# Performance work log

Measured on AMD Instinct MI355X. Metric: run time of the kernel, lower is better.

## Reference

```python
import jax, jax.numpy as jnp
import numpy as np

B, D, K, H, W = 2, 512, 32, 64, 64


def setup_inputs() -> dict:
    key = jax.random.key(0)
    k1, k2, k3 = jax.random.split(key, 3)
    X = jax.random.normal(k1, (B, D, H, W), dtype=jnp.float32)
    std1 = 1.0 / (K * D) ** 0.5
    codewords = jax.random.uniform(k2, (K, D), minval=-std1, maxval=std1, dtype=jnp.float32)
    scale = jax.random.uniform(k3, (D, K), minval=-1.0, maxval=0.0, dtype=jnp.float32)
    return {"X": X, "codewords": codewords, "scale": scale}


def reference(X, codewords, scale):
    # X: [B, D, H, W] -> x: [B, N, D], N = H*W
    Bv, Dv = X.shape[0], X.shape[1]
    x = X.reshape(Bv, Dv, -1).transpose(0, 2, 1)            # [B, N, D]
    # broadcast residual: x[b,n,d] - codewords[k,d], scaled per (d,k)
    residual = (x[:, :, :, None] - codewords.T) * scale     # [B, N, D, K]
    # soft assignment over K codewords
    Q = jax.nn.softmax(-0.5 * jnp.sum(residual * residual, axis=2), axis=2)  # [B, N, K]
    # weighted aggregation over N, normalized by per-codeword mass
    Z_num = jnp.einsum('bnk,bndk->bdk', Q, residual)        # [B, D, K]
    Z_ = Z_num / Q.sum(axis=1)[:, None, :]                  # [B, D, K]
    # L2-normalize along D
    Z = Z_ / jnp.sqrt(jnp.sum(Z_ * Z_, axis=1, keepdims=True))
    return (Z, Q)
```

## Files before the change

### kernel.cpp

```cpp
#include <hip/hip_runtime.h>
#include <math.h>

#define B_DIM 2
#define D_DIM 512
#define K_DIM 32
#define N_DIM 4096

__global__ __launch_bounds__(256, 2)
void k_dist_q(const float* __restrict__ X, const float* __restrict__ CW,
              const float* __restrict__ SC, float* __restrict__ Qout,
              float* __restrict__ nsq)
{
    __shared__ __align__(16) float xlds[16 * 516];
    __shared__ __align__(16) float red[16 * 16 * 36];

    const int tid = threadIdx.x;
    const int b  = blockIdx.x >> 8;
    const int n0 = (blockIdx.x & 255) << 4;
    const int dp = tid & 63;
    const int kp = tid >> 6;
    const int k0 = kp << 3;

    if (blockIdx.x == 0 && tid < 2 * K_DIM) nsq[tid] = 0.f;

    const float* xsrc = X + (size_t)b * D_DIM * N_DIM + n0;
#pragma unroll
    for (int j = 0; j < 8; ++j) {
        const int d  = (tid >> 2) + (j << 6);
        const int n4 = (tid & 3) << 2;
        float4 v = *(const float4*)(xsrc + (size_t)d * N_DIM + n4);
        xlds[(n4 + 0) * 516 + d] = v.x;
        xlds[(n4 + 1) * 516 + d] = v.y;
        xlds[(n4 + 2) * 516 + d] = v.z;
        xlds[(n4 + 3) * 516 + d] = v.w;
    }

    float cv[8][8];
#pragma unroll
    for (int kk = 0; kk < 8; ++kk) {
        const float* cr = CW + (k0 + kk) * D_DIM + (dp << 2);
        float4 c0 = *(const float4*)(cr);
        float4 c1 = *(const float4*)(cr + 256);
        cv[kk][0] = c0.x; cv[kk][1] = c0.y; cv[kk][2] = c0.z; cv[kk][3] = c0.w;
        cv[kk][4] = c1.x; cv[kk][5] = c1.y; cv[kk][6] = c1.z; cv[kk][7] = c1.w;
    }
    float Areg[8][8], Breg[8][8], ckp[8];
#pragma unroll
    for (int kk = 0; kk < 8; ++kk) ckp[kk] = 0.f;
#pragma unroll
    for (int dd = 0; dd < 8; ++dd) {
        const int d = (dd < 4) ? ((dp << 2) + dd) : (256 + (dp << 2) + (dd - 4));
        float4 s0 = *(const float4*)(SC + d * K_DIM + k0);
        float4 s1 = *(const float4*)(SC + d * K_DIM + k0 + 4);
        float sv[8] = {s0.x, s0.y, s0.z, s0.w, s1.x, s1.y, s1.z, s1.w};
#pragma unroll
        for (int kk = 0; kk < 8; ++kk) {
            float c = cv[kk][dd];
            float a = sv[kk] * sv[kk];
            Areg[dd][kk] = a;
            Breg[dd][kk] = -2.f * a * c;
            ckp[kk] = fmaf(a * c, c, ckp[kk]);
        }
    }
    __syncthreads();

#pragma unroll
    for (int n = 0; n < 16; ++n) {
        float dist[8];
#pragma unroll
        for (int kk = 0; kk < 8; ++kk) dist[kk] = ckp[kk];
        float4 xa = *(const float4*)(&xlds[n * 516 + (dp << 2)]);
        float4 xb = *(const float4*)(&xlds[n * 516 + (dp << 2) + 256]);
        float xv[8] = {xa.x, xa.y, xa.z, xa.w, xb.x, xb.y, xb.z, xb.w};
#pragma unroll
        for (int dd = 0; dd < 8; ++dd) {
            const float x  = xv[dd];
            const float x2 = x * x;
#pragma unroll
            for (int kk = 0; kk < 8; ++kk) {
                dist[kk] = fmaf(Areg[dd][kk], x2, dist[kk]);
                dist[kk] = fmaf(Breg[dd][kk], x,  dist[kk]);
            }
        }
#pragma unroll
        for (int kk = 0; kk < 8; ++kk) {
            dist[kk] += __shfl_xor(dist[kk], 32);
            dist[kk] += __shfl_xor(dist[kk], 16);
        }
        if (dp < 16) {
            float* r = &red[(n * 16 + dp) * 36 + k0];
            *(float4*)(r)     = make_float4(dist[0], dist[1], dist[2], dist[3]);
            *(float4*)(r + 4) = make_float4(dist[4], dist[5], dist[6], dist[7]);
        }
    }
    __syncthreads();

#pragma unroll
    for (int h = 0; h < 2; ++h) {
        const int n = (tid >> 5) + (h << 3);
        const int k = tid & 31;
        float dsum = 0.f;
#pragma unroll
        for (int i = 0; i < 16; ++i) dsum += red[(n * 16 + i) * 36 + k];
        float m = dsum;
#pragma unroll
        for (int mk = 16; mk >= 1; mk >>= 1)
            m = fminf(m, __shfl_xor(m, mk));
        float e = __expf(-0.5f * (dsum - m));
        float ssum = e;
#pragma unroll
        for (int mk = 16; mk >= 1; mk >>= 1)
            ssum += __shfl_xor(ssum, mk);
        Qout[((size_t)b * N_DIM + n0 + n) * K_DIM + k] = __fdividef(e, ssum);
    }
}

__global__ __launch_bounds__(256, 2)
void k_tpart(const float* __restrict__ X, const float* __restrict__ Qin,
             float* __restrict__ TP, float* __restrict__ Mpart)
{
    __shared__ __align__(16) float Xs[64 * 68];
    __shared__ __align__(16) float Qs[32 * 68];
    __shared__ __align__(16) float red4[4 * 64 * 36];
    __shared__ float mred[8][33];

    const int tid = threadIdx.x;
    const int bid = blockIdx.x;
    const int ns = bid & 31;
    const int dt = (bid >> 5) & 7;
    const int b  = bid >> 8;
    const int nsub = tid >> 5;
    const int dp = tid & 7;
    const int kp = (tid >> 3) & 3;
    const int wv = tid >> 6;

    float acc[8][8];
#pragma unroll
    for (int i = 0; i < 8; ++i)
#pragma unroll
        for (int j = 0; j < 8; ++j) acc[i][j] = 0.f;

    const float* xsrc = X + ((size_t)b * D_DIM + dt * 64) * N_DIM + ns * 128;
    const float* qsrc = Qin + ((size_t)b * N_DIM + ns * 128) * K_DIM;

    for (int ch = 0; ch < 2; ++ch) {
        __syncthreads();
#pragma unroll
        for (int i = 0; i < 4; ++i) {
            int flat4 = tid + (i << 8);
            int row = flat4 >> 4;
            int c4  = (flat4 & 15) << 2;
            float4 v = *(const float4*)(xsrc + (size_t)row * N_DIM + (ch << 6) + c4);
            *(float4*)(&Xs[row * 68 + c4]) = v;
        }
#pragma unroll
        for (int i = 0; i < 2; ++i) {
            int flat4 = tid + (i << 8);
            int nn = flat4 >> 3;
            int k4 = (flat4 & 7) << 2;
            float4 v = *(const float4*)(qsrc + ((ch << 6) + nn) * K_DIM + k4);
            Qs[(k4 + 0) * 68 + nn] = v.x;
            Qs[(k4 + 1) * 68 + nn] = v.y;
            Qs[(k4 + 2) * 68 + nn] = v.z;
            Qs[(k4 + 3) * 68 + nn] = v.w;
        }
        __syncthreads();
#pragma unroll
        for (int s = 0; s < 2; ++s) {
            const int nb = (nsub << 3) + (s << 2);
            float4 xr[8], qr[8];
#pragma unroll
            for (int i = 0; i < 8; ++i)
                xr[i] = *(const float4*)(&Xs[(dp + (i << 3)) * 68 + nb]);
#pragma unroll
            for (int j = 0; j < 8; ++j)
                qr[j] = *(const float4*)(&Qs[(kp + (j << 2)) * 68 + nb]);
#pragma unroll
            for (int i = 0; i < 8; ++i)
#pragma unroll
                for (int j = 0; j < 8; ++j) {
                    acc[i][j] = fmaf(xr[i].x, qr[j].x, acc[i][j]);
                    acc[i][j] = fmaf(xr[i].y, qr[j].y, acc[i][j]);
                    acc[i][j] = fmaf(xr[i].z, qr[j].z, acc[i][j]);
                    acc[i][j] = fmaf(xr[i].w, qr[j].w, acc[i][j]);
                }
        }
    }
    __syncthreads();
#pragma unroll
    for (int i = 0; i < 8; ++i)
#pragma unroll
        for (int j = 0; j < 8; ++j)
            acc[i][j] += __shfl_xor(acc[i][j], 32);
    if ((tid & 32) == 0) {
#pragma unroll
        for (int i = 0; i < 8; ++i)
#pragma unroll
            for (int j = 0; j < 8; ++j)
                red4[(wv * 64 + dp + (i << 3)) * 36 + kp + (j << 2)] = acc[i][j];
    }
    __syncthreads();
    float* dst = TP + (((size_t)ns * 2 + b) * D_DIM + dt * 64) * K_DIM;
#pragma unroll
    for (int e = 0; e < 8; ++e) {
        int flat = tid + (e << 8);
        int dl = flat >> 5;
        int k  = flat & 31;
        float s = red4[(0 * 64 + dl) * 36 + k] + red4[(1 * 64 + dl) * 36 + k]
                + red4[(2 * 64 + dl) * 36 + k] + red4[(3 * 64 + dl) * 36 + k];
        dst[dl * K_DIM + k] = s;
    }
    if (dt == 0) {
        const int k = tid & 31, g = tid >> 5;
        float qm = 0.f;
#pragma unroll
        for (int n = 0; n < 16; ++n)
            qm += qsrc[(g * 16 + n) * K_DIM + k];
        mred[g][k] = qm;
        __syncthreads();
        if (tid < K_DIM) {
            float t = 0.f;
#pragma unroll
            for (int i = 0; i < 8; ++i) t += mred[i][tid];
            Mpart[(ns * B_DIM + b) * K_DIM + tid] = t;
        }
    }
}

__global__ __launch_bounds__(256)
void k_zpre(const float* __restrict__ TP, const float* __restrict__ Mpart,
            const float* __restrict__ CW, const float* __restrict__ SC,
            float* __restrict__ Ztmp, float* __restrict__ nsq)
{
    __shared__ float part[8][33];
    const int tid = threadIdx.x;
    const int b  = blockIdx.x >> 6;
    const int ds = blockIdx.x & 63;
    const int d  = (ds << 3) + (tid >> 5);
    const int k  = tid & 31;
    float sum = 0.f;
#pragma unroll
    for (int ns = 0; ns < 32; ++ns)
        sum += TP[(((size_t)ns * 2 + b) * D_DIM + d) * K_DIM + k];
    float m = 0.f;
#pragma unroll
    for (int ns = 0; ns < 32; ++ns)
        m += Mpart[(ns * B_DIM + b) * K_DIM + k];
    float c = CW[k * D_DIM + d];
    float s = SC[d * K_DIM + k];
    float z = s * (sum / m - c);
    Ztmp[((size_t)b * D_DIM + d) * K_DIM + k] = z;
    part[tid >> 5][k] = z * z;
    __syncthreads();
    if (tid < K_DIM) {
        float t = 0.f;
#pragma unroll
        for (int i = 0; i < 8; ++i) t += part[i][tid];
        atomicAdd(&nsq[b * K_DIM + tid], t);
    }
}

__global__ __launch_bounds__(256)
void k_zfin(const float* __restrict__ Ztmp, const float* __restrict__ nsq,
            float* __restrict__ Z)
{
    const int tid = threadIdx.x;
    const int b  = blockIdx.x >> 6;
    const int ds = blockIdx.x & 63;
    const int d  = (ds << 3) + (tid >> 5);
    const int k  = tid & 31;
    const int idx = ((b * D_DIM) + d) * K_DIM + k;
    Z[idx] = Ztmp[idx] * rsqrtf(nsq[b * K_DIM + k]);
}

extern "C" void kernel_launch(void* const* d_in, const int* in_sizes, int n_in,
                              void* d_out, int out_size, void* d_ws, size_t ws_size,
                              hipStream_t stream)
{
    const float* X  = (const float*)d_in[0];
    const float* CW = (const float*)d_in[1];
    const float* SC = (const float*)d_in[2];
    float* Z = (float*)d_out;
    float* Q = (float*)d_out + B_DIM * D_DIM * K_DIM;

    float* W    = (float*)d_ws;
    float* nsq  = W;
    float* Mpart= W + 64;
    float* TP   = W + 64 + 2048;
    float* ZT   = TP + 32 * B_DIM * D_DIM * K_DIM;

    k_dist_q<<<512, 256, 0, stream>>>(X, CW, SC, Q, nsq);
    k_tpart <<<512, 256, 0, stream>>>(X, Q, TP, Mpart);
    k_zpre  <<<128, 256, 0, stream>>>(TP, Mpart, CW, SC, ZT, nsq);
    k_zfin  <<<128, 256, 0, stream>>>(ZT, nsq, Z);
}
```

Before: 96.88 us.

## Fuse Z finalization via grid-wide spin barrier and atomically accumulate T partials

Raises k_dist_q to 512 threads, with each wave handling 4 codewords instead of 8. That kernel now also zeroes the T accumulator and writes per-block Q mass partials, which removes the Mpart work from the second kernel. k_tacc accumulates its partial products into a single T buffer with atomicAdd instead of writing 32 slices. k_zpre and k_zfin are merged into one kernel that uses an atomic counter spin barrier to wait for the global norm sums. This drops one launch and the 32-way TP reduction, but adds atomic contention and relies on all 128 blocks being co-resident for the spin barrier.

```diff
diff --git a/kernel.cpp b/kernel.cpp
--- a/kernel.cpp
+++ b/kernel.cpp
@@ -6,10 +6,13 @@
 #define K_DIM 32
 #define N_DIM 4096
 
-__global__ __launch_bounds__(256, 2)
+#define WS_T_OFF   128
+#define WS_MP_OFF  (128 + B_DIM * D_DIM * K_DIM)
+
+__global__ __launch_bounds__(512, 4)
 void k_dist_q(const float* __restrict__ X, const float* __restrict__ CW,
               const float* __restrict__ SC, float* __restrict__ Qout,
-              float* __restrict__ nsq)
+              float* __restrict__ W)
 {
     __shared__ __align__(16) float xlds[16 * 516];
     __shared__ __align__(16) float red[16 * 16 * 36];
@@ -18,15 +21,19 @@
     const int b  = blockIdx.x >> 8;
     const int n0 = (blockIdx.x & 255) << 4;
     const int dp = tid & 63;
-    const int kp = tid >> 6;
-    const int k0 = kp << 3;
-
-    if (blockIdx.x == 0 && tid < 2 * K_DIM) nsq[tid] = 0.f;
+    const int kw = tid >> 6;
+    const int k0 = kw << 2;
+
+    {
+        float* T = W + WS_T_OFF;
+        if (tid < 64) T[(blockIdx.x << 6) + tid] = 0.f;
+        if (blockIdx.x == 0 && tid >= 64 && tid < 129) W[tid - 64] = 0.f;
+    }
 
     const float* xsrc = X + (size_t)b * D_DIM * N_DIM + n0;
 #pragma unroll
-    for (int j = 0; j < 8; ++j) {
-        const int d  = (tid >> 2) + (j << 6);
+    for (int j = 0; j < 4; ++j) {
+        const int d  = (tid >> 2) + (j << 7);
         const int n4 = (tid & 3) << 2;
         float4 v = *(const float4*)(xsrc + (size_t)d * N_DIM + n4);
         xlds[(n4 + 0) * 516 + d] = v.x;
@@ -35,40 +42,38 @@
         xlds[(n4 + 3) * 516 + d] = v.w;
     }
 
-    float cv[8][8];
-#pragma unroll
-    for (int kk = 0; kk < 8; ++kk) {
+    float cv[4][8];
+#pragma unroll
+    for (int kk = 0; kk < 4; ++kk) {
         const float* cr = CW + (k0 + kk) * D_DIM + (dp << 2);
         float4 c0 = *(const float4*)(cr);
         float4 c1 = *(const float4*)(cr + 256);
         cv[kk][0] = c0.x; cv[kk][1] = c0.y; cv[kk][2] = c0.z; cv[kk][3] = c0.w;
         cv[kk][4] = c1.x; cv[kk][5] = c1.y; cv[kk][6] = c1.z; cv[kk][7] = c1.w;
     }
-    float Areg[8][8], Breg[8][8], ckp[8];
-#pragma unroll
-    for (int kk = 0; kk < 8; ++kk) ckp[kk] = 0.f;
+    float Areg[8][4], Breg[8][4], ckp[4];
+#pragma unroll
+    for (int kk = 0; kk < 4; ++kk) ckp[kk] = 0.f;
 #pragma unroll
     for (int dd = 0; dd < 8; ++dd) {
         const int d = (dd < 4) ? ((dp << 2) + dd) : (256 + (dp << 2) + (dd - 4));
-        float4 s0 = *(const float4*)(SC + d * K_DIM + k0);
-        float4 s1 = *(const float4*)(SC + d * K_DIM + k0 + 4);
-        float sv[8] = {s0.x, s0.y, s0.z, s0.w, s1.x, s1.y, s1.z, s1.w};
-#pragma unroll
-        for (int kk = 0; kk < 8; ++kk) {
+        float4 s4 = *(const float4*)(SC + d * K_DIM + k0);
+        float sv[4] = {s4.x, s4.y, s4.z, s4.w};
+#pragma unroll
+        for (int kk = 0; kk < 4; ++kk) {
             float c = cv[kk][dd];
             float a = sv[kk] * sv[kk];
+            float t = a * c;
             Areg[dd][kk] = a;
-            Breg[dd][kk] = -2.f * a * c;
-            ckp[kk] = fmaf(a * c, c, ckp[kk]);
+            Breg[dd][kk] = -2.f * t;
+            ckp[kk] = fmaf(t, c, ckp[kk]);
         }
     }
     __syncthreads();
 
 #pragma unroll
     for (int n = 0; n < 16; ++n) {
-        float dist[8];
-#pragma unroll
-        for (int kk = 0; kk < 8; ++kk) dist[kk] = ckp[kk];
+        float dist[4] = {ckp[0], ckp[1], ckp[2], ckp[3]};
         float4 xa = *(const float4*)(&xlds[n * 516 + (dp << 2)]);
         float4 xb = *(const float4*)(&xlds[n * 516 + (dp << 2) + 256]);
         float xv[8] = {xa.x, xa.y, xa.z, xa.w, xb.x, xb.y, xb.z, xb.w};
@@ -77,52 +82,57 @@
             const float x  = xv[dd];
             const float x2 = x * x;
 #pragma unroll
-            for (int kk = 0; kk < 8; ++kk) {
+            for (int kk = 0; kk < 4; ++kk) {
                 dist[kk] = fmaf(Areg[dd][kk], x2, dist[kk]);
                 dist[kk] = fmaf(Breg[dd][kk], x,  dist[kk]);
             }
         }
 #pragma unroll
-        for (int kk = 0; kk < 8; ++kk) {
+        for (int kk = 0; kk < 4; ++kk) {
             dist[kk] += __shfl_xor(dist[kk], 32);
             dist[kk] += __shfl_xor(dist[kk], 16);
         }
-        if (dp < 16) {
-            float* r = &red[(n * 16 + dp) * 36 + k0];
-            *(float4*)(r)     = make_float4(dist[0], dist[1], dist[2], dist[3]);
-            *(float4*)(r + 4) = make_float4(dist[4], dist[5], dist[6], dist[7]);
-        }
-    }
-    __syncthreads();
-
-#pragma unroll
-    for (int h = 0; h < 2; ++h) {
-        const int n = (tid >> 5) + (h << 3);
-        const int k = tid & 31;
-        float dsum = 0.f;
-#pragma unroll
-        for (int i = 0; i < 16; ++i) dsum += red[(n * 16 + i) * 36 + k];
-        float m = dsum;
-#pragma unroll
-        for (int mk = 16; mk >= 1; mk >>= 1)
-            m = fminf(m, __shfl_xor(m, mk));
-        float e = __expf(-0.5f * (dsum - m));
-        float ssum = e;
-#pragma unroll
-        for (int mk = 16; mk >= 1; mk >>= 1)
-            ssum += __shfl_xor(ssum, mk);
-        Qout[((size_t)b * N_DIM + n0 + n) * K_DIM + k] = __fdividef(e, ssum);
+        if (dp < 16)
+            *(float4*)(&red[(n * 16 + dp) * 36 + k0]) =
+                make_float4(dist[0], dist[1], dist[2], dist[3]);
+    }
+    __syncthreads();
+
+    const int n = tid >> 5;
+    const int k = tid & 31;
+    float dsum = 0.f;
+#pragma unroll
+    for (int i = 0; i < 16; ++i) dsum += red[(n * 16 + i) * 36 + k];
+    float m = dsum;
+#pragma unroll
+    for (int mk = 16; mk >= 1; mk >>= 1)
+        m = fminf(m, __shfl_xor(m, mk));
+    float e = __expf(-0.5f * (dsum - m));
+    float ssum = e;
+#pragma unroll
+    for (int mk = 16; mk >= 1; mk >>= 1)
+        ssum += __shfl_xor(ssum, mk);
+    float q = __fdividef(e, ssum);
+    Qout[((size_t)b * N_DIM + n0 + n) * K_DIM + k] = q;
+
+    __syncthreads();
+    xlds[n * 33 + k] = q;
+    __syncthreads();
+    if (tid < K_DIM) {
+        float t = 0.f;
+#pragma unroll
+        for (int i = 0; i < 16; ++i) t += xlds[i * 33 + tid];
+        W[WS_MP_OFF + blockIdx.x * K_DIM + tid] = t;
     }
 }
 
 __global__ __launch_bounds__(256, 2)
-void k_tpart(const float* __restrict__ X, const float* __restrict__ Qin,
-             float* __restrict__ TP, float* __restrict__ Mpart)
+void k_tacc(const float* __restrict__ X, const float* __restrict__ Qin,
+            float* __restrict__ W)
 {
     __shared__ __align__(16) float Xs[64 * 68];
     __shared__ __align__(16) float Qs[32 * 68];
     __shared__ __align__(16) float red4[4 * 64 * 36];
-    __shared__ float mred[8][33];
 
     const int tid = threadIdx.x;
     const int bid = blockIdx.x;
@@ -200,7 +210,7 @@
                 red4[(wv * 64 + dp + (i << 3)) * 36 + kp + (j << 2)] = acc[i][j];
     }
     __syncthreads();
-    float* dst = TP + (((size_t)ns * 2 + b) * D_DIM + dt * 64) * K_DIM;
+    float* T = W + WS_T_OFF + (((size_t)b * D_DIM + dt * 64) * K_DIM);
 #pragma unroll
     for (int e = 0; e < 8; ++e) {
         int flat = tid + (e << 8);
@@ -208,69 +218,72 @@
         int k  = flat & 31;
         float s = red4[(0 * 64 + dl) * 36 + k] + red4[(1 * 64 + dl) * 36 + k]
                 + red4[(2 * 64 + dl) * 36 + k] + red4[(3 * 64 + dl) * 36 + k];
-        dst[dl * K_DIM + k] = s;
-    }
-    if (dt == 0) {
-        const int k = tid & 31, g = tid >> 5;
-        float qm = 0.f;
-#pragma unroll
-        for (int n = 0; n < 16; ++n)
-            qm += qsrc[(g * 16 + n) * K_DIM + k];
-        mred[g][k] = qm;
-        __syncthreads();
-        if (tid < K_DIM) {
-            float t = 0.f;
-#pragma unroll
-            for (int i = 0; i < 8; ++i) t += mred[i][tid];
-            Mpart[(ns * B_DIM + b) * K_DIM + tid] = t;
-        }
+        atomicAdd(&T[dl * K_DIM + k], s);
     }
 }
 
 __global__ __launch_bounds__(256)
-void k_zpre(const float* __restrict__ TP, const float* __restrict__ Mpart,
-            const float* __restrict__ CW, const float* __restrict__ SC,
-            float* __restrict__ Ztmp, float* __restrict__ nsq)
+void k_zfin(const float* __restrict__ CW, const float* __restrict__ SC,
+            float* __restrict__ W, float* __restrict__ Z)
 {
+    __shared__ float mred[8][33];
+    __shared__ float Msh[K_DIM];
     __shared__ float part[8][33];
+
     const int tid = threadIdx.x;
     const int b  = blockIdx.x >> 6;
     const int ds = blockIdx.x & 63;
-    const int d  = (ds << 3) + (tid >> 5);
+    const int g  = tid >> 5;
+    const int d  = (ds << 3) + g;
     const int k  = tid & 31;
-    float sum = 0.f;
-#pragma unroll
-    for (int ns = 0; ns < 32; ++ns)
-        sum += TP[(((size_t)ns * 2 + b) * D_DIM + d) * K_DIM + k];
-    float m = 0.f;
-#pragma unroll
-    for (int ns = 0; ns < 32; ++ns)
-        m += Mpart[(ns * B_DIM + b) * K_DIM + k];
-    float c = CW[k * D_DIM + d];
-    float s = SC[d * K_DIM + k];
-    float z = s * (sum / m - c);
-    Ztmp[((size_t)b * D_DIM + d) * K_DIM + k] = z;
-    part[tid >> 5][k] = z * z;
+
+    float* nsq = W;
+    int*   cnt = (int*)(W + 64);
+    const float* T  = W + WS_T_OFF;
+    const float* Mp = W + WS_MP_OFF;
+
+    float pm = 0.f;
+#pragma unroll
+    for (int i = 0; i < 32; ++i)
+        pm += Mp[((b << 8) + (g << 5) + i) * K_DIM + k];
+    mred[g][k] = pm;
     __syncthreads();
     if (tid < K_DIM) {
         float t = 0.f;
 #pragma unroll
-        for (int i = 0; i < 8; ++i) t += part[i][tid];
-        atomicAdd(&nsq[b * K_DIM + tid], t);
-    }
-}
-
-__global__ __launch_bounds__(256)
-void k_zfin(const float* __restrict__ Ztmp, const float* __restrict__ nsq,
-            float* __restrict__ Z)
-{
-    const int tid = threadIdx.x;
-    const int b  = blockIdx.x >> 6;
-    const int ds = blockIdx.x & 63;
-    const int d  = (ds << 3) + (tid >> 5);
-    const int k  = tid & 31;
-    const int idx = ((b * D_DIM) + d) * K_DIM + k;
-    Z[idx] = Ztmp[idx] * rsqrtf(nsq[b * K_DIM + k]);
+        for (int i = 0; i < 8; ++i) t += mred[i][tid];
+        Msh[tid] = t;
+    }
+    __syncthreads();
+    const float m = Msh[k];
+
+    const float t = T[((size_t)(b * D_DIM + d)) * K_DIM + k];
+    const float c = CW[k * D_DIM + d];
+    const float s = SC[d * K_DIM + k];
+    const float z = s * (t / m - c);
+
+    part[g][k] = z * z;
+    __syncthreads();
+    if (tid < K_DIM) {
+        float q = 0.f;
+#pragma unroll
+        for (int i = 0; i < 8; ++i) q += part[i][tid];
+        atomicAdd(&nsq[(b << 5) + tid], q);
+    }
+
+    __threadfence();
+    __syncthreads();
+    if (tid == 0) {
+        __hip_atomic_fetch_add(cnt, 1, __ATOMIC_ACQ_REL, __HIP_MEMORY_SCOPE_AGENT);
+        while (__hip_atomic_load(cnt, __ATOMIC_ACQUIRE, __HIP_MEMORY_SCOPE_AGENT)
+               < (int)gridDim.x)
+            __builtin_amdgcn_s_sleep(2);
+    }
+    __syncthreads();
+
+    const float nv = __hip_atomic_load(&nsq[(b << 5) + k], __ATOMIC_RELAXED,
+                                       __HIP_MEMORY_SCOPE_AGENT);
+    Z[((size_t)(b * D_DIM + d)) * K_DIM + k] = z * rsqrtf(nv);
 }
 
 extern "C" void kernel_launch(void* const* d_in, const int* in_sizes, int n_in,
@@ -282,15 +295,9 @@
     const float* SC = (const float*)d_in[2];
     float* Z = (float*)d_out;
     float* Q = (float*)d_out + B_DIM * D_DIM * K_DIM;
-
-    float* W    = (float*)d_ws;
-    float* nsq  = W;
-    float* Mpart= W + 64;
-    float* TP   = W + 64 + 2048;
-    float* ZT   = TP + 32 * B_DIM * D_DIM * K_DIM;
-
-    k_dist_q<<<512, 256, 0, stream>>>(X, CW, SC, Q, nsq);
-    k_tpart <<<512, 256, 0, stream>>>(X, Q, TP, Mpart);
-    k_zpre  <<<128, 256, 0, stream>>>(TP, Mpart, CW, SC, ZT, nsq);
-    k_zfin  <<<128, 256, 0, stream>>>(ZT, nsq, Z);
+    float* W = (float*)d_ws;
+
+    k_dist_q<<<512, 512, 0, stream>>>(X, CW, SC, Q, W);
+    k_tacc  <<<512, 256, 0, stream>>>(X, Q, W);
+    k_zfin  <<<128, 256, 0, stream>>>(CW, SC, W, Z);
 }
```

Result: slower. 107.0 us (+10.5%).
